# Optimization experiments

Hardware: AMD Instinct MI355X
Metric: run time of the kernel (lower is better)

## Reference

```python
import jax, jax.numpy as jnp
import numpy as np
import math

SCALED = True
SUBSEQUENT_MASK = True
B, SQ, SK, D, DV = 8, 2048, 2048, 1024, 1024


def _build_mask(query_lens, key_lens, sq, sk, causal):
    # (B, Sq, Sk) boolean validity mask: rows >= q_len and cols >= k_len are masked.
    qm = jnp.arange(sq)[None, :, None] < query_lens[:, None, None]
    km = jnp.arange(sk)[None, None, :] < key_lens[:, None, None]
    mask = qm & km
    if causal:
        mask = mask & (jnp.arange(sk)[None, None, :] <= jnp.arange(sq)[None, :, None])
    return mask


def _masked_softmax(scores, mask):
    # Stable masked softmax; fully-masked rows yield exactly 0 (matches the
    # original's NaN -> 0 replacement) without producing NaNs.
    neg = jnp.finfo(scores.dtype).min
    s = jnp.where(mask, scores, neg)
    m = jnp.max(s, axis=-1, keepdims=True)
    e = jnp.where(mask, jnp.exp(s - m), jnp.zeros((), scores.dtype))
    denom = jnp.sum(e, axis=-1, keepdims=True)
    return e / jnp.where(denom == 0, jnp.ones((), scores.dtype), denom)


def setup_inputs() -> dict:
    key = jax.random.key(0)
    kq, kk, kv, kql, kkl = jax.random.split(key, 5)
    return {
        "queries": jax.random.normal(kq, (B, SQ, D), dtype=jnp.float32),
        "keys": jax.random.normal(kk, (B, SK, D), dtype=jnp.float32),
        "values": jax.random.normal(kv, (B, SK, DV), dtype=jnp.float32),
        "query_lens": jax.random.randint(kql, (B,), 1, SQ + 1),
        "key_lens": jax.random.randint(kkl, (B,), 1, SK + 1),
    }


def reference(queries, keys, values, query_lens, key_lens):
    # scores: (B, Sq, Sk)
    scores = jnp.einsum("bqd,bkd->bqk", queries, keys)
    if SCALED:
        scores = scores / math.sqrt(queries.shape[2])
    mask = _build_mask(query_lens, key_lens, queries.shape[1], keys.shape[1], SUBSEQUENT_MASK)
    weights = _masked_softmax(scores, mask)
    context = jnp.einsum("bqk,bkv->bqv", weights, values)
    return (context, weights)
```

## Files before the change

kernel.cpp:

```cpp
#include <hip/hip_runtime.h>
#include <hip/hip_bf16.h>

#define B_   8
#define SQ_  2048
#define SK_  2048
#define D_   1024
#define DV_  1024

typedef __bf16 bf16;
typedef __attribute__((ext_vector_type(4))) __bf16 bf16x4;
typedef __attribute__((ext_vector_type(8))) __bf16 bf16x8;
typedef __attribute__((ext_vector_type(4))) float  f32x4;

__global__ __launch_bounds__(256)
void scores_kernel(const float* __restrict__ Q, const float* __restrict__ K,
                   const int* __restrict__ qlens, const int* __restrict__ klens,
                   float* __restrict__ Wout)
{
    const int b  = blockIdx.z;
    const int q0 = blockIdx.y * 128;
    const int k0 = blockIdx.x * 128;
    if (k0 > q0 + 127) return;
    const int qlen = qlens[b], klen = klens[b];
    if (q0 >= qlen || k0 >= klen) return;

    __shared__ __align__(16) bf16 Qs[128][72];
    __shared__ __align__(16) bf16 Ks[128][72];

    const int tid  = threadIdx.x;
    const int lane = tid & 63;
    const int w    = tid >> 6;
    const int wq   = w >> 1, wk = w & 1;

    const float* Qb = Q + (size_t)b * SQ_ * D_;
    const float* Kb = K + (size_t)b * SK_ * D_;

    f32x4 acc[4][4] = {};

    for (int d0 = 0; d0 < D_; d0 += 64) {
        #pragma unroll
        for (int i = 0; i < 8; ++i) {
            int s   = tid + i * 256;
            int row = s >> 4;
            int c4  = (s & 15) << 2;
            const float4 qv = *(const float4*)(Qb + (size_t)(q0 + row) * D_ + d0 + c4);
            const float4 kv = *(const float4*)(Kb + (size_t)(k0 + row) * D_ + d0 + c4);
            bf16x4 qb = { (bf16)qv.x, (bf16)qv.y, (bf16)qv.z, (bf16)qv.w };
            bf16x4 kb = { (bf16)kv.x, (bf16)kv.y, (bf16)kv.z, (bf16)kv.w };
            *(bf16x4*)&Qs[row][c4] = qb;
            *(bf16x4*)&Ks[row][c4] = kb;
        }
        __syncthreads();
        #pragma unroll
        for (int kk = 0; kk < 2; ++kk) {
            const int koff = kk * 32 + ((lane >> 4) << 3);
            bf16x8 a[4], bb[4];
            #pragma unroll
            for (int m = 0; m < 4; ++m)
                a[m] = *(const bf16x8*)&Qs[64 * wq + 16 * m + (lane & 15)][koff];
            #pragma unroll
            for (int n = 0; n < 4; ++n)
                bb[n] = *(const bf16x8*)&Ks[64 * wk + 16 * n + (lane & 15)][koff];
            #pragma unroll
            for (int m = 0; m < 4; ++m)
                #pragma unroll
                for (int n = 0; n < 4; ++n)
                    acc[m][n] = __builtin_amdgcn_mfma_f32_16x16x32_bf16(a[m], bb[n], acc[m][n], 0, 0, 0);
        }
        __syncthreads();
    }

    float* Wb = Wout + (size_t)b * SQ_ * SK_;
    const int rb = q0 + 64 * wq + ((lane >> 4) << 2);
    const int cb = k0 + 64 * wk + (lane & 15);
    #pragma unroll
    for (int m = 0; m < 4; ++m)
        #pragma unroll
        for (int n = 0; n < 4; ++n)
            #pragma unroll
            for (int r = 0; r < 4; ++r)
                Wb[(size_t)(rb + 16 * m + r) * SK_ + (cb + 16 * n)] = acc[m][n][r] * 0.03125f;
}

__global__ __launch_bounds__(256)
void softmax_kernel(const int* __restrict__ qlens, const int* __restrict__ klens,
                    float* __restrict__ W)
{
    const int bq = blockIdx.x;
    const int b  = bq >> 11;
    const int q  = bq & 2047;
    const int qlen = qlens[b], klen = klens[b];
    int kmax = 0;
    if (q < qlen) kmax = min(klen, q + 1);

    float4* row = (float4*)(W + (size_t)bq * SK_);
    const int tid = threadIdx.x;

    float4 x[2];
    float m = -INFINITY;
    #pragma unroll
    for (int i = 0; i < 2; ++i) {
        int v4 = tid + i * 256;
        x[i] = row[v4];
        int kb = v4 << 2;
        float* xe = (float*)&x[i];
        #pragma unroll
        for (int e = 0; e < 4; ++e) {
            if (kb + e >= kmax) xe[e] = -INFINITY;
            m = fmaxf(m, xe[e]);
        }
    }
    #pragma unroll
    for (int off = 32; off > 0; off >>= 1) m = fmaxf(m, __shfl_xor(m, off, 64));
    __shared__ float red[4];
    if ((tid & 63) == 0) red[tid >> 6] = m;
    __syncthreads();
    m = fmaxf(fmaxf(red[0], red[1]), fmaxf(red[2], red[3]));
    __syncthreads();

    float sum = 0.f;
    #pragma unroll
    for (int i = 0; i < 2; ++i) {
        float* xe = (float*)&x[i];
        #pragma unroll
        for (int e = 0; e < 4; ++e) {
            float ev = (xe[e] == -INFINITY) ? 0.f : __expf(xe[e] - m);
            xe[e] = ev;
            sum += ev;
        }
    }
    #pragma unroll
    for (int off = 32; off > 0; off >>= 1) sum += __shfl_xor(sum, off, 64);
    if ((tid & 63) == 0) red[tid >> 6] = sum;
    __syncthreads();
    sum = red[0] + red[1] + red[2] + red[3];

    const float inv = (sum > 0.f) ? (1.f / sum) : 0.f;
    #pragma unroll
    for (int i = 0; i < 2; ++i) {
        float* xe = (float*)&x[i];
        float4 o = { xe[0] * inv, xe[1] * inv, xe[2] * inv, xe[3] * inv };
        row[tid + i * 256] = o;
    }
}

__global__ __launch_bounds__(256)
void context_kernel(const float* __restrict__ W, const float* __restrict__ V,
                    const int* __restrict__ klens, float* __restrict__ Out)
{
    const int b  = blockIdx.z;
    const int q0 = blockIdx.y * 128;
    const int n0 = blockIdx.x * 128;
    const int klen = klens[b];
    const int kend = min(q0 + 128, (klen + 63) & ~63);

    __shared__ __align__(16) bf16 Ws[128][72];
    __shared__ __align__(16) bf16 Vs[128][72];

    const int tid  = threadIdx.x;
    const int lane = tid & 63;
    const int w    = tid >> 6;
    const int wq   = w >> 1, wn = w & 1;

    const float* Wb = W + (size_t)b * SQ_ * SK_;
    const float* Vb = V + (size_t)b * SK_ * DV_;

    f32x4 acc[4][4] = {};

    for (int kk0 = 0; kk0 < kend; kk0 += 64) {
        #pragma unroll
        for (int i = 0; i < 8; ++i) {
            int s   = tid + i * 256;
            int row = s >> 4;
            int c4  = (s & 15) << 2;
            const float4 wv = *(const float4*)(Wb + (size_t)(q0 + row) * SK_ + kk0 + c4);
            bf16x4 wb = { (bf16)wv.x, (bf16)wv.y, (bf16)wv.z, (bf16)wv.w };
            *(bf16x4*)&Ws[row][c4] = wb;
        }
        #pragma unroll
        for (int i = 0; i < 4; ++i) {
            int t   = tid + i * 256;
            int n   = t & 127;
            int oct = t >> 7;
            float v[8];
            #pragma unroll
            for (int j = 0; j < 8; ++j)
                v[j] = Vb[(size_t)(kk0 + oct * 8 + j) * DV_ + n0 + n];
            bf16x8 vb = { (bf16)v[0], (bf16)v[1], (bf16)v[2], (bf16)v[3],
                          (bf16)v[4], (bf16)v[5], (bf16)v[6], (bf16)v[7] };
            *(bf16x8*)&Vs[n][oct * 8] = vb;
        }
        __syncthreads();
        #pragma unroll
        for (int kk = 0; kk < 2; ++kk) {
            const int koff = kk * 32 + ((lane >> 4) << 3);
            bf16x8 a[4], bb[4];
            #pragma unroll
            for (int m = 0; m < 4; ++m)
                a[m] = *(const bf16x8*)&Ws[64 * wq + 16 * m + (lane & 15)][koff];
            #pragma unroll
            for (int n = 0; n < 4; ++n)
                bb[n] = *(const bf16x8*)&Vs[64 * wn + 16 * n + (lane & 15)][koff];
            #pragma unroll
            for (int m = 0; m < 4; ++m)
                #pragma unroll
                for (int n = 0; n < 4; ++n)
                    acc[m][n] = __builtin_amdgcn_mfma_f32_16x16x32_bf16(a[m], bb[n], acc[m][n], 0, 0, 0);
        }
        __syncthreads();
    }

    float* Ob = Out + (size_t)b * SQ_ * DV_;
    const int rb = q0 + 64 * wq + ((lane >> 4) << 2);
    const int cb = n0 + 64 * wn + (lane & 15);
    #pragma unroll
    for (int m = 0; m < 4; ++m)
        #pragma unroll
        for (int n = 0; n < 4; ++n)
            #pragma unroll
            for (int r = 0; r < 4; ++r)
                Ob[(size_t)(rb + 16 * m + r) * DV_ + (cb + 16 * n)] = acc[m][n][r];
}

extern "C" void kernel_launch(void* const* d_in, const int* in_sizes, int n_in,
                              void* d_out, int out_size, void* d_ws, size_t ws_size,
                              hipStream_t stream) {
    (void)in_sizes; (void)n_in; (void)out_size; (void)d_ws; (void)ws_size;
    const float* Q     = (const float*)d_in[0];
    const float* K     = (const float*)d_in[1];
    const float* V     = (const float*)d_in[2];
    const int*   qlens = (const int*)d_in[3];
    const int*   klens = (const int*)d_in[4];

    float* ctx = (float*)d_out;
    float* wts = ctx + (size_t)B_ * SQ_ * DV_;

    dim3 g1(SK_ / 128, SQ_ / 128, B_);
    scores_kernel<<<g1, 256, 0, stream>>>(Q, K, qlens, klens, wts);

    softmax_kernel<<<dim3(B_ * SQ_), 256, 0, stream>>>(qlens, klens, wts);

    dim3 g3(DV_ / 128, SQ_ / 128, B_);
    context_kernel<<<g3, 256, 0, stream>>>(wts, V, klens, ctx);
}
```

Measured before the change: 509.5 us.

## Double-buffer GEMM tiles with register prefetch and use 512-thread blocks

The scores and context GEMM kernels now prefetch the next 64-wide K tile into registers while MFMAs run on the current shared-memory buffer, then write it to a second LDS buffer. Each kernel runs with 512 threads, so each of the 8 waves computes a 32x64 sub-tile instead of 64x64. The goal is to hide global-load latency behind compute. The cost is doubled LDS use, higher register pressure from the prefetch buffers and __launch_bounds__(512,4), and less reuse of operands within each wave. Separately, the softmax kernel no longer loads masked score elements beyond kmax, which saves memory reads on short or causal rows.

Result: faster. 472.3 us (-7.3%).

```diff
diff --git a/kernel.cpp b/kernel.cpp
--- a/kernel.cpp
+++ b/kernel.cpp
@@ -12,7 +12,7 @@
 typedef __attribute__((ext_vector_type(8))) __bf16 bf16x8;
 typedef __attribute__((ext_vector_type(4))) float  f32x4;
 
-__global__ __launch_bounds__(256)
+__global__ __launch_bounds__(512, 4)
 void scores_kernel(const float* __restrict__ Q, const float* __restrict__ K,
                    const int* __restrict__ qlens, const int* __restrict__ klens,
                    float* __restrict__ Wout)
@@ -24,8 +24,8 @@
     const int qlen = qlens[b], klen = klens[b];
     if (q0 >= qlen || k0 >= klen) return;
 
-    __shared__ __align__(16) bf16 Qs[128][72];
-    __shared__ __align__(16) bf16 Ks[128][72];
+    __shared__ __align__(16) bf16 Qs[2][128][72];
+    __shared__ __align__(16) bf16 Ks[2][128][72];
 
     const int tid  = threadIdx.x;
     const int lane = tid & 63;
@@ -35,46 +35,66 @@
     const float* Qb = Q + (size_t)b * SQ_ * D_;
     const float* Kb = K + (size_t)b * SK_ * D_;
 
-    f32x4 acc[4][4] = {};
-
-    for (int d0 = 0; d0 < D_; d0 += 64) {
-        #pragma unroll
-        for (int i = 0; i < 8; ++i) {
-            int s   = tid + i * 256;
-            int row = s >> 4;
-            int c4  = (s & 15) << 2;
-            const float4 qv = *(const float4*)(Qb + (size_t)(q0 + row) * D_ + d0 + c4);
-            const float4 kv = *(const float4*)(Kb + (size_t)(k0 + row) * D_ + d0 + c4);
-            bf16x4 qb = { (bf16)qv.x, (bf16)qv.y, (bf16)qv.z, (bf16)qv.w };
-            bf16x4 kb = { (bf16)kv.x, (bf16)kv.y, (bf16)kv.z, (bf16)kv.w };
-            *(bf16x4*)&Qs[row][c4] = qb;
-            *(bf16x4*)&Ks[row][c4] = kb;
-        }
-        __syncthreads();
+    float4 qreg[4], kreg[4];
+    int srow[4], sc4[4];
+    #pragma unroll
+    for (int i = 0; i < 4; ++i) {
+        int s = tid + i * 512;
+        srow[i] = s >> 4;
+        sc4[i]  = (s & 15) << 2;
+    }
+
+    auto load_tile = [&](int d0) {
+        #pragma unroll
+        for (int i = 0; i < 4; ++i) {
+            qreg[i] = *(const float4*)(Qb + (size_t)(q0 + srow[i]) * D_ + d0 + sc4[i]);
+            kreg[i] = *(const float4*)(Kb + (size_t)(k0 + srow[i]) * D_ + d0 + sc4[i]);
+        }
+    };
+    auto store_tile = [&](int buf) {
+        #pragma unroll
+        for (int i = 0; i < 4; ++i) {
+            bf16x4 qb = { (bf16)qreg[i].x, (bf16)qreg[i].y, (bf16)qreg[i].z, (bf16)qreg[i].w };
+            bf16x4 kb = { (bf16)kreg[i].x, (bf16)kreg[i].y, (bf16)kreg[i].z, (bf16)kreg[i].w };
+            *(bf16x4*)&Qs[buf][srow[i]][sc4[i]] = qb;
+            *(bf16x4*)&Ks[buf][srow[i]][sc4[i]] = kb;
+        }
+    };
+
+    f32x4 acc[2][4] = {};
+
+    load_tile(0);
+    store_tile(0);
+    __syncthreads();
+
+    for (int it = 0; it < 16; ++it) {
+        const int cur = it & 1;
+        if (it < 15) load_tile((it + 1) * 64);
         #pragma unroll
         for (int kk = 0; kk < 2; ++kk) {
             const int koff = kk * 32 + ((lane >> 4) << 3);
-            bf16x8 a[4], bb[4];
-            #pragma unroll
-            for (int m = 0; m < 4; ++m)
-                a[m] = *(const bf16x8*)&Qs[64 * wq + 16 * m + (lane & 15)][koff];
+            bf16x8 a[2], bb[4];
+            #pragma unroll
+            for (int m = 0; m < 2; ++m)
+                a[m] = *(const bf16x8*)&Qs[cur][32 * wq + 16 * m + (lane & 15)][koff];
             #pragma unroll
             for (int n = 0; n < 4; ++n)
-                bb[n] = *(const bf16x8*)&Ks[64 * wk + 16 * n + (lane & 15)][koff];
-            #pragma unroll
-            for (int m = 0; m < 4; ++m)
+                bb[n] = *(const bf16x8*)&Ks[cur][64 * wk + 16 * n + (lane & 15)][koff];
+            #pragma unroll
+            for (int m = 0; m < 2; ++m)
                 #pragma unroll
                 for (int n = 0; n < 4; ++n)
                     acc[m][n] = __builtin_amdgcn_mfma_f32_16x16x32_bf16(a[m], bb[n], acc[m][n], 0, 0, 0);
         }
+        if (it < 15) store_tile(1 - cur);
         __syncthreads();
     }
 
     float* Wb = Wout + (size_t)b * SQ_ * SK_;
-    const int rb = q0 + 64 * wq + ((lane >> 4) << 2);
+    const int rb = q0 + 32 * wq + ((lane >> 4) << 2);
     const int cb = k0 + 64 * wk + (lane & 15);
     #pragma unroll
-    for (int m = 0; m < 4; ++m)
+    for (int m = 0; m < 2; ++m)
         #pragma unroll
         for (int n = 0; n < 4; ++n)
             #pragma unroll
@@ -101,8 +121,9 @@
     #pragma unroll
     for (int i = 0; i < 2; ++i) {
         int v4 = tid + i * 256;
-        x[i] = row[v4];
         int kb = v4 << 2;
+        if (kb < kmax) x[i] = row[v4];
+        else           x[i] = make_float4(-INFINITY, -INFINITY, -INFINITY, -INFINITY);
         float* xe = (float*)&x[i];
         #pragma unroll
         for (int e = 0; e < 4; ++e) {
@@ -144,7 +165,7 @@
     }
 }
 
-__global__ __launch_bounds__(256)
+__global__ __launch_bounds__(512, 4)
 void context_kernel(const float* __restrict__ W, const float* __restrict__ V,
                     const int* __restrict__ klens, float* __restrict__ Out)
 {
@@ -153,9 +174,10 @@
     const int n0 = blockIdx.x * 128;
     const int klen = klens[b];
     const int kend = min(q0 + 128, (klen + 63) & ~63);
-
-    __shared__ __align__(16) bf16 Ws[128][72];
-    __shared__ __align__(16) bf16 Vs[128][72];
+    const int nk   = kend >> 6;
+
+    __shared__ __align__(16) bf16 Ws[2][128][72];
+    __shared__ __align__(16) bf16 Vs[2][128][72];
 
     const int tid  = threadIdx.x;
     const int lane = tid & 63;
@@ -165,56 +187,80 @@
     const float* Wb = W + (size_t)b * SQ_ * SK_;
     const float* Vb = V + (size_t)b * SK_ * DV_;
 
-    f32x4 acc[4][4] = {};
-
-    for (int kk0 = 0; kk0 < kend; kk0 += 64) {
-        #pragma unroll
-        for (int i = 0; i < 8; ++i) {
-            int s   = tid + i * 256;
-            int row = s >> 4;
-            int c4  = (s & 15) << 2;
-            const float4 wv = *(const float4*)(Wb + (size_t)(q0 + row) * SK_ + kk0 + c4);
-            bf16x4 wb = { (bf16)wv.x, (bf16)wv.y, (bf16)wv.z, (bf16)wv.w };
-            *(bf16x4*)&Ws[row][c4] = wb;
-        }
+    float4 wreg[4];
+    float  vreg[2][8];
+    int srow[4], sc4[4], vn[2], voct[2];
+    #pragma unroll
+    for (int i = 0; i < 4; ++i) {
+        int s = tid + i * 512;
+        srow[i] = s >> 4;
+        sc4[i]  = (s & 15) << 2;
+    }
+    #pragma unroll
+    for (int i = 0; i < 2; ++i) {
+        int t = tid + i * 512;
+        vn[i]   = t & 127;
+        voct[i] = t >> 7;
+    }
+
+    auto load_tile = [&](int kk0) {
+        #pragma unroll
+        for (int i = 0; i < 4; ++i)
+            wreg[i] = *(const float4*)(Wb + (size_t)(q0 + srow[i]) * SK_ + kk0 + sc4[i]);
+        #pragma unroll
+        for (int i = 0; i < 2; ++i)
+            #pragma unroll
+            for (int j = 0; j < 8; ++j)
+                vreg[i][j] = Vb[(size_t)(kk0 + voct[i] * 8 + j) * DV_ + n0 + vn[i]];
+    };
+    auto store_tile = [&](int buf) {
         #pragma unroll
         for (int i = 0; i < 4; ++i) {
-            int t   = tid + i * 256;
-            int n   = t & 127;
-            int oct = t >> 7;
-            float v[8];
-            #pragma unroll
-            for (int j = 0; j < 8; ++j)
-                v[j] = Vb[(size_t)(kk0 + oct * 8 + j) * DV_ + n0 + n];
-            bf16x8 vb = { (bf16)v[0], (bf16)v[1], (bf16)v[2], (bf16)v[3],
-                          (bf16)v[4], (bf16)v[5], (bf16)v[6], (bf16)v[7] };
-            *(bf16x8*)&Vs[n][oct * 8] = vb;
-        }
-        __syncthreads();
+            bf16x4 wb = { (bf16)wreg[i].x, (bf16)wreg[i].y, (bf16)wreg[i].z, (bf16)wreg[i].w };
+            *(bf16x4*)&Ws[buf][srow[i]][sc4[i]] = wb;
+        }
+        #pragma unroll
+        for (int i = 0; i < 2; ++i) {
+            bf16x8 vb = { (bf16)vreg[i][0], (bf16)vreg[i][1], (bf16)vreg[i][2], (bf16)vreg[i][3],
+                          (bf16)vreg[i][4], (bf16)vreg[i][5], (bf16)vreg[i][6], (bf16)vreg[i][7] };
+            *(bf16x8*)&Vs[buf][vn[i]][voct[i] * 8] = vb;
+        }
+    };
+
+    f32x4 acc[2][4] = {};
+
+    load_tile(0);
+    store_tile(0);
+    __syncthreads();
+
+    for (int it = 0; it < nk; ++it) {
+        const int cur = it & 1;
+        if (it + 1 < nk) load_tile((it + 1) * 64);
         #pragma unroll
         for (int kk = 0; kk < 2; ++kk) {
             const int koff = kk * 32 + ((lane >> 4) << 3);
-            bf16x8 a[4], bb[4];
-            #pragma unroll
-            for (int m = 0; m < 4; ++m)
-                a[m] = *(const bf16x8*)&Ws[64 * wq + 16 * m + (lane & 15)][koff];
+            bf16x8 a[2], bb[4];
+            #pragma unroll
+            for (int m = 0; m < 2; ++m)
+                a[m] = *(const bf16x8*)&Ws[cur][32 * wq + 16 * m + (lane & 15)][koff];
             #pragma unroll
             for (int n = 0; n < 4; ++n)
-                bb[n] = *(const bf16x8*)&Vs[64 * wn + 16 * n + (lane & 15)][koff];
-            #pragma unroll
-            for (int m = 0; m < 4; ++m)
+                bb[n] = *(const bf16x8*)&Vs[cur][64 * wn + 16 * n + (lane & 15)][koff];
+            #pragma unroll
+            for (int m = 0; m < 2; ++m)
                 #pragma unroll
                 for (int n = 0; n < 4; ++n)
                     acc[m][n] = __builtin_amdgcn_mfma_f32_16x16x32_bf16(a[m], bb[n], acc[m][n], 0, 0, 0);
         }
+        if (it + 1 < nk) store_tile(1 - cur);
         __syncthreads();
     }
 
     float* Ob = Out + (size_t)b * SQ_ * DV_;
-    const int rb = q0 + 64 * wq + ((lane >> 4) << 2);
+    const int rb = q0 + 32 * wq + ((lane >> 4) << 2);
     const int cb = n0 + 64 * wn + (lane & 15);
     #pragma unroll
-    for (int m = 0; m < 4; ++m)
+    for (int m = 0; m < 2; ++m)
         #pragma unroll
         for (int n = 0; n < 4; ++n)
             #pragma unroll
@@ -236,10 +282,10 @@
     float* wts = ctx + (size_t)B_ * SQ_ * DV_;
 
     dim3 g1(SK_ / 128, SQ_ / 128, B_);
-    scores_kernel<<<g1, 256, 0, stream>>>(Q, K, qlens, klens, wts);
+    scores_kernel<<<g1, 512, 0, stream>>>(Q, K, qlens, klens, wts);
 
     softmax_kernel<<<dim3(B_ * SQ_), 256, 0, stream>>>(qlens, klens, wts);
 
     dim3 g3(DV_ / 128, SQ_ / 128, B_);
-    context_kernel<<<g3, 256, 0, stream>>>(wts, V, klens, ctx);
-}
+    context_kernel<<<g3, 512, 0, stream>>>(wts, V, klens, ctx);
+}
```
